# Performance work log

Measured on AMD Instinct MI355X. Metric: run time of the kernel, lower is better.

Reference implementation:

```python
import jax, jax.numpy as jnp
import numpy as np

N_NODES = 50000
N_EDGES = 1600000
IN_DIM = 128
HID_DIM = 128
OUT_DIM = 64


def setup_inputs() -> dict:
    key = jax.random.key(0)
    ks = jax.random.split(key, 10)
    n_feat = jax.random.normal(ks[0], (N_NODES, IN_DIM), dtype=jnp.float32)
    edge_weights = jax.random.uniform(ks[1], (N_EDGES, 1), dtype=jnp.float32)
    src = jax.random.randint(ks[2], (N_EDGES,), 0, N_NODES, dtype=jnp.int32)
    dst = jax.random.randint(ks[3], (N_EDGES,), 0, N_NODES, dtype=jnp.int32)
    # Linear(in*2, out) weights, torch layout [out_features, in_features]
    s1 = 1.0 / np.sqrt(2 * IN_DIM)
    s2 = 1.0 / np.sqrt(2 * HID_DIM)
    W1 = jax.random.uniform(ks[4], (HID_DIM, 2 * IN_DIM), jnp.float32, -s1, s1)
    b1 = jax.random.uniform(ks[5], (HID_DIM,), jnp.float32, -s1, s1)
    W2 = jax.random.uniform(ks[6], (HID_DIM, 2 * HID_DIM), jnp.float32, -s2, s2)
    b2 = jax.random.uniform(ks[7], (HID_DIM,), jnp.float32, -s2, s2)
    W3 = jax.random.uniform(ks[8], (OUT_DIM, 2 * HID_DIM), jnp.float32, -s2, s2)
    b3 = jax.random.uniform(ks[9], (OUT_DIM,), jnp.float32, -s2, s2)
    return {"n_feat": n_feat, "edge_weights": edge_weights, "src": src,
            "dst": dst, "W1": W1, "b1": b1, "W2": W2, "b2": b2,
            "W3": W3, "b3": b3}


def reference(n_feat, edge_weights, src, dst, W1, b1, W2, b2, W3, b3):
    N = n_feat.shape[0]
    E = src.shape[0]
    # in-degree for mean aggregation (DGL mean gives 0 for isolated nodes)
    deg = jax.ops.segment_sum(jnp.ones((E,), n_feat.dtype), dst, num_segments=N)
    inv_deg = jnp.where(deg > 0, 1.0 / jnp.maximum(deg, 1.0), 0.0)[:, None]

    def layer(h, W, b):
        m = h[src] * edge_weights                        # [E, d] gather-multiply
        agg = jax.ops.segment_sum(m, dst, num_segments=N) * inv_deg  # mean scatter
        z = jnp.concatenate([agg, h], axis=-1) @ W.T + b
        return jax.nn.relu(z)

    h = layer(n_feat, W1, b1)
    h = layer(h, W2, b2)
    h = layer(h, W3, b3)
    return h
```

## Files before the change

kernel.cpp:

```cpp
#include <hip/hip_runtime.h>

#define NN 50000
#define NE 1600000
#define NPART 196
#define PSZ 256

typedef _Float16 f16;
typedef __attribute__((ext_vector_type(8))) _Float16 f16x8;
typedef __attribute__((ext_vector_type(4))) float f32x4;


__global__ __launch_bounds__(256) void part_count(const int* __restrict__ dst,
                                                  unsigned* __restrict__ pcount, int E) {
    __shared__ unsigned hist[NPART];
    for (int i = threadIdx.x; i < NPART; i += 256) hist[i] = 0;
    __syncthreads();
    for (int e = blockIdx.x * 256 + threadIdx.x; e < E; e += gridDim.x * 256)
        atomicAdd(&hist[((unsigned)dst[e]) >> 8], 1u);
    __syncthreads();
    for (int i = threadIdx.x; i < NPART; i += 256) {
        unsigned c = hist[i];
        if (c) atomicAdd(&pcount[i], c);
    }
}

__global__ void part_scan(const unsigned* __restrict__ pcount,
                          unsigned* __restrict__ poff, unsigned* __restrict__ pcursor) {
    const int t = threadIdx.x;
    const int lane = t & 63, wid = t >> 6;
    __shared__ unsigned wsum[4];
    unsigned v = (t < NPART) ? pcount[t] : 0u;
    unsigned x = v;
    #pragma unroll
    for (int s = 1; s < 64; s <<= 1) {
        unsigned tt = __shfl_up(x, s, 64);
        if (lane >= s) x += tt;
    }
    if (lane == 63) wsum[wid] = x;
    __syncthreads();
    if (t == 0) { unsigned s = 0; for (int k = 0; k < 4; ++k) { unsigned tt = wsum[k]; wsum[k] = s; s += tt; } }
    __syncthreads();
    unsigned excl = x - v + wsum[wid];
    if (t <= NPART) { poff[t] = excl; pcursor[t] = excl; }
}

__global__ __launch_bounds__(512) void bucket_scatter(
    const int* __restrict__ dst, const int* __restrict__ src, const float* __restrict__ ew,
    unsigned* __restrict__ pcursor, unsigned long long* __restrict__ tmp, int E) {
    __shared__ unsigned hist[NPART];
    __shared__ unsigned gbase[NPART];
    const int chunk = blockIdx.x * 8192;
    for (int i = threadIdx.x; i < NPART; i += 512) hist[i] = 0;
    __syncthreads();
    #pragma unroll
    for (int r = 0; r < 16; ++r) {
        int e = chunk + threadIdx.x + r * 512;
        if (e < E) atomicAdd(&hist[((unsigned)dst[e]) >> 8], 1u);
    }
    __syncthreads();
    for (int i = threadIdx.x; i < NPART; i += 512) {
        unsigned c = hist[i];
        gbase[i] = c ? atomicAdd(&pcursor[i], c) : 0u;
        hist[i] = 0;
    }
    __syncthreads();
    #pragma unroll
    for (int r = 0; r < 16; ++r) {
        int e = chunk + threadIdx.x + r * 512;
        if (e < E) {
            unsigned d = (unsigned)dst[e];
            unsigned part = d >> 8;
            unsigned rank = atomicAdd(&hist[part], 1u);
            unsigned long long rec =
                ((unsigned long long)__float_as_uint(ew[e]) << 32)
              | ((unsigned long long)(d & 0xffu) << 16)
              | (unsigned)src[e];
            tmp[gbase[part] + rank] = rec;
        }
    }
}

__global__ __launch_bounds__(256) void part_sort(
    const unsigned long long* __restrict__ tmp, const unsigned* __restrict__ poff,
    unsigned long long* __restrict__ edges, unsigned* __restrict__ off,
    float* __restrict__ invdeg, int N) {
    __shared__ unsigned hist[PSZ];
    __shared__ unsigned excl[PSZ];
    __shared__ unsigned wsum[4];
    const int b = blockIdx.x;
    const unsigned e0 = poff[b], e1 = poff[b + 1];
    const int t = threadIdx.x;
    hist[t] = 0;
    __syncthreads();
    for (unsigned i = e0 + t; i < e1; i += 256)
        atomicAdd(&hist[(unsigned)(tmp[i] >> 16) & 0xffu], 1u);
    __syncthreads();
    const unsigned v = hist[t];
    const int lane = t & 63, wid = t >> 6;
    unsigned x = v;
    #pragma unroll
    for (int s = 1; s < 64; s <<= 1) {
        unsigned tt = __shfl_up(x, s, 64);
        if (lane >= s) x += tt;
    }
    if (lane == 63) wsum[wid] = x;
    __syncthreads();
    if (t == 0) { unsigned s = 0; for (int k = 0; k < 4; ++k) { unsigned tt = wsum[k]; wsum[k] = s; s += tt; } }
    __syncthreads();
    const unsigned ex = x - v + wsum[wid];
    excl[t] = ex;
    const int node = b * PSZ + t;
    if (node < N) {
        off[node] = e0 + ex;
        invdeg[node] = v ? 1.0f / (float)v : 0.0f;
    }
    if (b == NPART - 1 && t == 0) off[N] = e1;
    hist[t] = 0;
    __syncthreads();
    for (unsigned i = e0 + t; i < e1; i += 256) {
        unsigned long long rec = tmp[i];
        unsigned doff = (unsigned)(rec >> 16) & 0xffu;
        unsigned r = atomicAdd(&hist[doff], 1u);
        edges[e0 + excl[doff] + r] = (rec & 0xffffffff00000000ull) | (rec & 0xffffull);
    }
}


__global__ __launch_bounds__(256) void pack_x(const float* __restrict__ in,
                                              f16* __restrict__ out, int n8) {
    int i = blockIdx.x * 256 + threadIdx.x;
    if (i < n8) {
        float4 a = ((const float4*)in)[i * 2];
        float4 b = ((const float4*)in)[i * 2 + 1];
        f16x8 h;
        h[0] = (f16)a.x; h[1] = (f16)a.y; h[2] = (f16)a.z; h[3] = (f16)a.w;
        h[4] = (f16)b.x; h[5] = (f16)b.y; h[6] = (f16)b.z; h[7] = (f16)b.w;
        ((f16x8*)out)[i] = h;
    }
}


template <int OUTH>
__global__ __launch_bounds__(256) void gemm_mfma(
    const f16* __restrict__ X, const float* __restrict__ W,
    const float* __restrict__ bias,
    f16* __restrict__ Pout,
    float* __restrict__ Qout,
    int N)
{
    const int tile = blockIdx.x * 64;
    const int colbase = blockIdx.y * 64;
    const int t = threadIdx.x;
    const int lane = t & 63;
    const int wv = t >> 6;

    __shared__ f16 Xs[64 * 128];
    __shared__ f16 Ws[64 * 128];

    #pragma unroll
    for (int i = 0; i < 4; ++i) {
        int row = i * 16 + (t >> 4);
        int chunk = t & 15;
        int v = tile + row;
        uint4 val = make_uint4(0u, 0u, 0u, 0u);
        if (v < N) val = ((const uint4*)(X + (size_t)v * 128))[chunk];
        ((uint4*)Xs)[row * 16 + (chunk ^ (row & 7))] = val;
    }
    const int isq = (colbase >= OUTH);
    #pragma unroll
    for (int i = 0; i < 4; ++i) {
        int row = i * 16 + (t >> 4);
        int chunk = t & 15;
        int c = colbase + row;
        const float* wsrc = W + (size_t)(isq ? c - OUTH : c) * 256 + (isq ? 128 : 0) + chunk * 8;
        float4 wa = *(const float4*)wsrc;
        float4 wb = *(const float4*)(wsrc + 4);
        f16x8 wh;
        wh[0] = (f16)wa.x; wh[1] = (f16)wa.y; wh[2] = (f16)wa.z; wh[3] = (f16)wa.w;
        wh[4] = (f16)wb.x; wh[5] = (f16)wb.y; wh[6] = (f16)wb.z; wh[7] = (f16)wb.w;
        ((f16x8*)Ws)[row * 16 + (chunk ^ (row & 7))] = wh;
    }
    __syncthreads();

    const int lr = lane & 15;
    const int kg = lane >> 4;
    f16x8 afrag[4];
    #pragma unroll
    for (int kb = 0; kb < 4; ++kb) {
        int row = wv * 16 + lr;
        afrag[kb] = ((const f16x8*)Xs)[row * 16 + ((kb * 4 + kg) ^ (row & 7))];
    }
    f32x4 acc[4];
    #pragma unroll
    for (int nt = 0; nt < 4; ++nt)
        #pragma unroll
        for (int j = 0; j < 4; ++j) acc[nt][j] = 0.0f;

    #pragma unroll
    for (int nt = 0; nt < 4; ++nt) {
        int col = nt * 16 + lr;
        #pragma unroll
        for (int kb = 0; kb < 4; ++kb) {
            f16x8 bfrag = ((const f16x8*)Ws)[col * 16 + ((kb * 4 + kg) ^ (col & 7))];
            acc[nt] = __builtin_amdgcn_mfma_f32_16x16x32_f16(afrag[kb], bfrag, acc[nt], 0, 0, 0);
        }
    }

    #pragma unroll
    for (int nt = 0; nt < 4; ++nt) {
        int c = colbase + nt * 16 + lr;
        #pragma unroll
        for (int j = 0; j < 4; ++j) {
            int v = tile + wv * 16 + kg * 4 + j;
            if (v >= N) continue;
            if (!isq) {
                Pout[(size_t)v * OUTH + c] = (f16)acc[nt][j];
            } else {
                int qc = c - OUTH;
                Qout[(size_t)v * OUTH + qc] = acc[nt][j] + bias[qc];
            }
        }
    }
}


#define UNPK(u, lo, hi) { union { unsigned uu; f16 hh[2]; } c_; c_.uu = (u); \
                          lo = (float)c_.hh[0]; hi = (float)c_.hh[1]; }

#define AGG_STEP(ED) {                                                          \
    unsigned srcv = (unsigned)(ED);                                             \
    float wvv = __uint_as_float((unsigned)((ED) >> 32));                        \
    const uint4 r = *(const uint4*)(P + (size_t)srcv * (LPR * 8) + lr * 8);     \
    float f0, f1, f2, f3, f4, f5, f6, f7;                                       \
    UNPK(r.x, f0, f1); UNPK(r.y, f2, f3); UNPK(r.z, f4, f5); UNPK(r.w, f6, f7); \
    a[0] = fmaf(f0, wvv, a[0]); a[1] = fmaf(f1, wvv, a[1]);                     \
    a[2] = fmaf(f2, wvv, a[2]); a[3] = fmaf(f3, wvv, a[3]);                     \
    a[4] = fmaf(f4, wvv, a[4]); a[5] = fmaf(f5, wvv, a[5]);                     \
    a[6] = fmaf(f6, wvv, a[6]); a[7] = fmaf(f7, wvv, a[7]); }

template <int LPR, bool F16OUT>
__global__ __launch_bounds__(256) void agg_fused(
    const f16* __restrict__ P,
    const float* __restrict__ Q,
    const unsigned long long* __restrict__ edges,
    const unsigned* __restrict__ off, const float* __restrict__ invdeg,
    void* __restrict__ outv)
{
    constexpr int DIM = LPR * 8;
    constexpr int G   = 64 / LPR;
    const int node = blockIdx.x * 4 + (threadIdx.x >> 6);
    const int lane = threadIdx.x & 63;
    const int g    = lane / LPR;
    const int lr   = lane % LPR;
    const unsigned s0 = off[node], s1 = off[node + 1];
    const unsigned deg = s1 - s0;
    const float inv = invdeg[node];

    float a[8];
    #pragma unroll
    for (int i = 0; i < 8; ++i) a[i] = 0.f;

    const unsigned long long* __restrict__ ep = edges + s0 + g;
    const unsigned nfull = deg / G;
    #pragma unroll 4
    for (unsigned it = 0; it < nfull; ++it) {
        unsigned long long ed = ep[(size_t)it * G];
        AGG_STEP(ed);
    }
    const unsigned tail = deg - nfull * G;
    if ((unsigned)g < tail) {
        unsigned long long ed = ep[(size_t)nfull * G];
        AGG_STEP(ed);
    }

    #pragma unroll
    for (int i = 0; i < 8; ++i) {
        a[i] += __shfl_xor(a[i], 32, 64);
        a[i] += __shfl_xor(a[i], 16, 64);
        if (LPR == 8) a[i] += __shfl_xor(a[i], 8, 64);
    }

    if (lane < LPR) {
        float4 q0 = *(const float4*)&Q[(size_t)node * DIM + lr * 8];
        float4 q1 = *(const float4*)&Q[(size_t)node * DIM + lr * 8 + 4];
        float o[8];
        o[0] = fmaxf(fmaf(a[0], inv, q0.x), 0.f);
        o[1] = fmaxf(fmaf(a[1], inv, q0.y), 0.f);
        o[2] = fmaxf(fmaf(a[2], inv, q0.z), 0.f);
        o[3] = fmaxf(fmaf(a[3], inv, q0.w), 0.f);
        o[4] = fmaxf(fmaf(a[4], inv, q1.x), 0.f);
        o[5] = fmaxf(fmaf(a[5], inv, q1.y), 0.f);
        o[6] = fmaxf(fmaf(a[6], inv, q1.z), 0.f);
        o[7] = fmaxf(fmaf(a[7], inv, q1.w), 0.f);
        if (F16OUT) {
            f16x8 h;
            #pragma unroll
            for (int i = 0; i < 8; ++i) h[i] = (f16)o[i];
            ((f16x8*)outv)[(size_t)node * (DIM / 8) + lr] = h;
        } else {
            float* out = (float*)outv;
            *(float4*)&out[(size_t)node * DIM + lr * 8]     = make_float4(o[0], o[1], o[2], o[3]);
            *(float4*)&out[(size_t)node * DIM + lr * 8 + 4] = make_float4(o[4], o[5], o[6], o[7]);
        }
    }
}


extern "C" void kernel_launch(void* const* d_in, const int* in_sizes, int n_in,
                              void* d_out, int out_size, void* d_ws, size_t ws_size,
                              hipStream_t stream) {
    const float* n_feat = (const float*)d_in[0];
    const float* ew     = (const float*)d_in[1];
    const int*   src    = (const int*)d_in[2];
    const int*   dst    = (const int*)d_in[3];
    const float* W1 = (const float*)d_in[4];
    const float* b1 = (const float*)d_in[5];
    const float* W2 = (const float*)d_in[6];
    const float* b2 = (const float*)d_in[7];
    const float* W3 = (const float*)d_in[8];
    const float* b3 = (const float*)d_in[9];

    const int N = NN, E = NE;

    uint8_t* w = (uint8_t*)d_ws;
    size_t o = 0;
    auto carve = [&](size_t bytes) { uint8_t* p = w + o; o += (bytes + 255) & ~(size_t)255; return p; };
    unsigned* pcount  = (unsigned*)carve((size_t)NPART * 4);
    unsigned* poff    = (unsigned*)carve((size_t)(NPART + 1) * 4);
    unsigned* pcursor = (unsigned*)carve((size_t)(NPART + 1) * 4);
    unsigned* off     = (unsigned*)carve((size_t)(N + 1) * 4);
    float*    invdeg  = (float*)   carve((size_t)N * 4);
    unsigned long long* edges = (unsigned long long*)carve((size_t)E * 8);
    f16*      Xf      = (f16*)     carve((size_t)N * 128 * 2);
    f16*      H       = (f16*)     carve((size_t)N * 128 * 2);
    f16*      P       = (f16*)     carve((size_t)N * 128 * 2);
    float*    Q       = (float*)   carve((size_t)N * 128 * 4);
    unsigned long long* tmp = (unsigned long long*)Q;

    float* OUT = (float*)d_out;

    hipMemsetAsync(pcount, 0, (size_t)NPART * 4, stream);
    part_count<<<392, 256, 0, stream>>>(dst, pcount, E);
    part_scan<<<1, 256, 0, stream>>>(pcount, poff, pcursor);
    bucket_scatter<<<(E + 8191) / 8192, 512, 0, stream>>>(dst, src, ew, pcursor, tmp, E);
    part_sort<<<NPART, 256, 0, stream>>>(tmp, poff, edges, off, invdeg, N);

    const int gx = (N + 63) / 64;

    pack_x<<<(N * 16 + 255) / 256, 256, 0, stream>>>(n_feat, Xf, N * 16);
    gemm_mfma<128><<<dim3(gx, 4), 256, 0, stream>>>(Xf, W1, b1, P, Q, N);
    agg_fused<16, true><<<N / 4, 256, 0, stream>>>(P, Q, edges, off, invdeg, H);

    gemm_mfma<128><<<dim3(gx, 4), 256, 0, stream>>>(H, W2, b2, P, Q, N);
    agg_fused<16, true><<<N / 4, 256, 0, stream>>>(P, Q, edges, off, invdeg, H);

    gemm_mfma<64><<<dim3(gx, 2), 256, 0, stream>>>(H, W3, b3, P, Q, N);
    agg_fused<8, false><<<N / 4, 256, 0, stream>>>(P, Q, edges, off, invdeg, OUT);
}
```

Baseline: 268.4 us.

## Compress edge records to 32 bits and aggregate over 32-column feature slabs

Edge records are packed into 32 bits: a 16-bit source index plus the edge weight rounded to fp16. This halves CSR edge traffic. The projected feature matrix P is stored slab-major in 32-column slabs, and aggregation launches one grid row per slab. Each pass then gathers only 64-byte rows from a much smaller working set that can stay cache-resident. The cost is that the edge list is re-read once per slab, the source index must fit in 16 bits (N=50000), and edge weights lose precision in fp16.

```diff
diff --git a/kernel.cpp b/kernel.cpp
--- a/kernel.cpp
+++ b/kernel.cpp
@@ -82,7 +82,7 @@
 
 __global__ __launch_bounds__(256) void part_sort(
     const unsigned long long* __restrict__ tmp, const unsigned* __restrict__ poff,
-    unsigned long long* __restrict__ edges, unsigned* __restrict__ off,
+    unsigned* __restrict__ edges, unsigned* __restrict__ off,
     float* __restrict__ invdeg, int N) {
     __shared__ unsigned hist[PSZ];
     __shared__ unsigned excl[PSZ];
@@ -121,7 +121,9 @@
         unsigned long long rec = tmp[i];
         unsigned doff = (unsigned)(rec >> 16) & 0xffu;
         unsigned r = atomicAdd(&hist[doff], 1u);
-        edges[e0 + excl[doff] + r] = (rec & 0xffffffff00000000ull) | (rec & 0xffffull);
+        union { f16 h; unsigned short u; } cw;
+        cw.h = (f16)__uint_as_float((unsigned)(rec >> 32));
+        edges[e0 + excl[doff] + r] = ((unsigned)cw.u << 16) | (unsigned)(rec & 0xffffull);
     }
 }
 
@@ -214,7 +216,8 @@
             int v = tile + wv * 16 + kg * 4 + j;
             if (v >= N) continue;
             if (!isq) {
-                Pout[(size_t)v * OUTH + c] = (f16)acc[nt][j];
+                int sl = c >> 5;
+                Pout[((size_t)sl * NN + v) * 32 + (c & 31)] = (f16)acc[nt][j];
             } else {
                 int qc = c - OUTH;
                 Qout[(size_t)v * OUTH + qc] = acc[nt][j] + bias[qc];
@@ -227,10 +230,11 @@
 #define UNPK(u, lo, hi) { union { unsigned uu; f16 hh[2]; } c_; c_.uu = (u); \
                           lo = (float)c_.hh[0]; hi = (float)c_.hh[1]; }
 
-#define AGG_STEP(ED) {                                                          \
-    unsigned srcv = (unsigned)(ED);                                             \
-    float wvv = __uint_as_float((unsigned)((ED) >> 32));                        \
-    const uint4 r = *(const uint4*)(P + (size_t)srcv * (LPR * 8) + lr * 8);     \
+#define AGG_STEP(REC) {                                                         \
+    unsigned srcv = (REC) & 0xffffu;                                            \
+    float wvv; { union { unsigned short u; f16 h; } cw;                         \
+                 cw.u = (unsigned short)((REC) >> 16); wvv = (float)cw.h; }     \
+    const uint4 r = *(const uint4*)(Pb + (size_t)srcv * 32 + lr * 8);           \
     float f0, f1, f2, f3, f4, f5, f6, f7;                                       \
     UNPK(r.x, f0, f1); UNPK(r.y, f2, f3); UNPK(r.z, f4, f5); UNPK(r.w, f6, f7); \
     a[0] = fmaf(f0, wvv, a[0]); a[1] = fmaf(f1, wvv, a[1]);                     \
@@ -238,51 +242,53 @@
     a[4] = fmaf(f4, wvv, a[4]); a[5] = fmaf(f5, wvv, a[5]);                     \
     a[6] = fmaf(f6, wvv, a[6]); a[7] = fmaf(f7, wvv, a[7]); }
 
-template <int LPR, bool F16OUT>
-__global__ __launch_bounds__(256) void agg_fused(
+template <int NS, bool F16OUT>
+__global__ __launch_bounds__(256) void agg_slab(
     const f16* __restrict__ P,
     const float* __restrict__ Q,
-    const unsigned long long* __restrict__ edges,
+    const unsigned* __restrict__ edges,
     const unsigned* __restrict__ off, const float* __restrict__ invdeg,
     void* __restrict__ outv)
 {
-    constexpr int DIM = LPR * 8;
-    constexpr int G   = 64 / LPR;
+    constexpr int DIM = NS * 32;
+    const int slab = blockIdx.y;
     const int node = blockIdx.x * 4 + (threadIdx.x >> 6);
     const int lane = threadIdx.x & 63;
-    const int g    = lane / LPR;
-    const int lr   = lane % LPR;
+    const int g    = lane >> 2;
+    const int lr   = lane & 3;
     const unsigned s0 = off[node], s1 = off[node + 1];
     const unsigned deg = s1 - s0;
     const float inv = invdeg[node];
+    const f16* __restrict__ Pb = P + (size_t)slab * NN * 32;
 
     float a[8];
     #pragma unroll
     for (int i = 0; i < 8; ++i) a[i] = 0.f;
 
-    const unsigned long long* __restrict__ ep = edges + s0 + g;
-    const unsigned nfull = deg / G;
-    #pragma unroll 4
+    const unsigned* __restrict__ ep = edges + s0 + g;
+    const unsigned nfull = deg >> 4;
+    #pragma unroll 2
     for (unsigned it = 0; it < nfull; ++it) {
-        unsigned long long ed = ep[(size_t)it * G];
-        AGG_STEP(ed);
-    }
-    const unsigned tail = deg - nfull * G;
-    if ((unsigned)g < tail) {
-        unsigned long long ed = ep[(size_t)nfull * G];
-        AGG_STEP(ed);
+        unsigned rec = ep[(size_t)it * 16];
+        AGG_STEP(rec);
+    }
+    if ((unsigned)g < (deg & 15u)) {
+        unsigned rec = ep[(size_t)nfull * 16];
+        AGG_STEP(rec);
     }
 
     #pragma unroll
     for (int i = 0; i < 8; ++i) {
         a[i] += __shfl_xor(a[i], 32, 64);
         a[i] += __shfl_xor(a[i], 16, 64);
-        if (LPR == 8) a[i] += __shfl_xor(a[i], 8, 64);
-    }
-
-    if (lane < LPR) {
-        float4 q0 = *(const float4*)&Q[(size_t)node * DIM + lr * 8];
-        float4 q1 = *(const float4*)&Q[(size_t)node * DIM + lr * 8 + 4];
+        a[i] += __shfl_xor(a[i], 8, 64);
+        a[i] += __shfl_xor(a[i], 4, 64);
+    }
+
+    if (lane < 4) {
+        const int cb = slab * 32 + lr * 8;
+        float4 q0 = *(const float4*)&Q[(size_t)node * DIM + cb];
+        float4 q1 = *(const float4*)&Q[(size_t)node * DIM + cb + 4];
         float o[8];
         o[0] = fmaxf(fmaf(a[0], inv, q0.x), 0.f);
         o[1] = fmaxf(fmaf(a[1], inv, q0.y), 0.f);
@@ -296,11 +302,11 @@
             f16x8 h;
             #pragma unroll
             for (int i = 0; i < 8; ++i) h[i] = (f16)o[i];
-            ((f16x8*)outv)[(size_t)node * (DIM / 8) + lr] = h;
+            *(f16x8*)((f16*)outv + (size_t)node * DIM + cb) = h;
         } else {
             float* out = (float*)outv;
-            *(float4*)&out[(size_t)node * DIM + lr * 8]     = make_float4(o[0], o[1], o[2], o[3]);
-            *(float4*)&out[(size_t)node * DIM + lr * 8 + 4] = make_float4(o[4], o[5], o[6], o[7]);
+            *(float4*)&out[(size_t)node * DIM + cb]     = make_float4(o[0], o[1], o[2], o[3]);
+            *(float4*)&out[(size_t)node * DIM + cb + 4] = make_float4(o[4], o[5], o[6], o[7]);
         }
     }
 }
@@ -330,7 +336,7 @@
     unsigned* pcursor = (unsigned*)carve((size_t)(NPART + 1) * 4);
     unsigned* off     = (unsigned*)carve((size_t)(N + 1) * 4);
     float*    invdeg  = (float*)   carve((size_t)N * 4);
-    unsigned long long* edges = (unsigned long long*)carve((size_t)E * 8);
+    unsigned* edges   = (unsigned*)carve((size_t)E * 4);
     f16*      Xf      = (f16*)     carve((size_t)N * 128 * 2);
     f16*      H       = (f16*)     carve((size_t)N * 128 * 2);
     f16*      P       = (f16*)     carve((size_t)N * 128 * 2);
@@ -349,11 +355,11 @@
 
     pack_x<<<(N * 16 + 255) / 256, 256, 0, stream>>>(n_feat, Xf, N * 16);
     gemm_mfma<128><<<dim3(gx, 4), 256, 0, stream>>>(Xf, W1, b1, P, Q, N);
-    agg_fused<16, true><<<N / 4, 256, 0, stream>>>(P, Q, edges, off, invdeg, H);
+    agg_slab<4, true><<<dim3(N / 4, 4), 256, 0, stream>>>(P, Q, edges, off, invdeg, H);
 
     gemm_mfma<128><<<dim3(gx, 4), 256, 0, stream>>>(H, W2, b2, P, Q, N);
-    agg_fused<16, true><<<N / 4, 256, 0, stream>>>(P, Q, edges, off, invdeg, H);
+    agg_slab<4, true><<<dim3(N / 4, 4), 256, 0, stream>>>(P, Q, edges, off, invdeg, H);
 
     gemm_mfma<64><<<dim3(gx, 2), 256, 0, stream>>>(H, W3, b3, P, Q, N);
-    agg_fused<8, false><<<N / 4, 256, 0, stream>>>(P, Q, edges, off, invdeg, OUT);
-}
+    agg_slab<2, false><<<dim3(N / 4, 2), 256, 0, stream>>>(P, Q, edges, off, invdeg, OUT);
+}
```

Measured after the change: 327.0 us. 1.22x slower.
